# Kernel tuning notes

Measured on AMD Instinct MI355X. Metric: run time of the kernel, lower is better.

The kernel has to match this reference:

```python
import jax, jax.numpy as jnp
import numpy as np


def setup_inputs() -> dict:
    key = jax.random.key(0)
    ks = jax.random.split(key, 7)
    OUT, IN, K = 4096, 4096, 2048
    U_STORED, VT_STORED = 512, 1024  # int(0.5*(K//2+1)), int(0.5*(IN//2+1))
    return {
        "x": jax.random.normal(ks[0], (1024, IN), dtype=jnp.float32),
        "U_real": jax.random.normal(ks[1], (OUT, U_STORED), dtype=jnp.float32) * 0.01,
        "U_imag": jax.random.normal(ks[2], (OUT, U_STORED), dtype=jnp.float32) * 0.01,
        "S": jax.random.normal(ks[3], (K,), dtype=jnp.float32) * 0.02,
        "Vt_real": jax.random.normal(ks[4], (K, VT_STORED), dtype=jnp.float32) * 0.01,
        "Vt_imag": jax.random.normal(ks[5], (K, VT_STORED), dtype=jnp.float32) * 0.01,
        "bias": jnp.zeros((OUT,), dtype=jnp.float32),
    }


def _decompress(coeffs_real, coeffs_imag, n):
    # Zero-pad truncated rfft coefficients back to n//2+1, then inverse rfft.
    c = jax.lax.complex(coeffs_real, coeffs_imag)
    num_unique = n // 2 + 1
    pad = num_unique - c.shape[-1]
    if pad > 0:
        c = jnp.pad(c, ((0, 0), (0, pad)))
    elif pad < 0:
        c = c[..., :num_unique]
    return jnp.fft.irfft(c, n=n, axis=-1)


def reference(x, U_real, U_imag, S, Vt_real, Vt_imag, bias):
    k_rank = S.shape[0]
    in_features = x.shape[-1]
    U = _decompress(U_real, U_imag, k_rank)            # (out, k)
    Vh = _decompress(Vt_real, Vt_imag, in_features)    # (k, in)
    W = (U * S[None, :]) @ Vh                          # (out, in) reconstructed weight
    return x @ W.T + bias                              # F.linear(x, W, bias)
```

## Files before the change

### kernel.cpp

```cpp
#include <hip/hip_runtime.h>
#include <math.h>
#include <stdint.h>

#define PI2 6.28318530717958647692f

typedef __bf16 bf16x8 __attribute__((ext_vector_type(8)));
typedef float f32x4 __attribute__((ext_vector_type(4)));

typedef __attribute__((address_space(1))) const void gvoid_t;
typedef __attribute__((address_space(3))) void lvoid_t;

__device__ __forceinline__ void g2l16(const void* g, void* l) {
    __builtin_amdgcn_global_load_lds(
        reinterpret_cast<gvoid_t*>(reinterpret_cast<uintptr_t>(g)),
        reinterpret_cast<lvoid_t*>(reinterpret_cast<uintptr_t>(l)),
        16, 0, 0);
}

__device__ __forceinline__ short f2bf(float f) {
    unsigned u = __float_as_uint(f);
    u += 0x7FFFu + ((u >> 16) & 1u);
    return (short)(u >> 16);
}

__device__ __forceinline__ unsigned pack2bf(float a, float b) {
    return (unsigned)(unsigned short)f2bf(a) |
           ((unsigned)(unsigned short)f2bf(b) << 16);
}

__device__ __forceinline__ float bflo(unsigned v) { return __uint_as_float(v << 16); }
__device__ __forceinline__ float bfhi(unsigned v) { return __uint_as_float(v & 0xFFFF0000u); }

__device__ __forceinline__ int xcd_swizzle(int blk, int G) {
    return (blk & 7) * (G >> 3) + (blk >> 3);
}

__global__ __launch_bounds__(256) void aux_all8(
    const float* __restrict__ x,
    const float* __restrict__ Ur, const float* __restrict__ Ui,
    const float* __restrict__ S,
    const float* __restrict__ Vr, const float* __restrict__ Vi,
    short* __restrict__ xe, short* __restrict__ xo,
    short* __restrict__ B1f, short* __restrict__ Vcat,
    short* __restrict__ B2, short* __restrict__ Ucat)
{
    unsigned i8 = (blockIdx.x * 256u + threadIdx.x) * 8u;
    if (i8 < 2097152u) {
        unsigned i = i8;
        int r = i >> 11, j0 = i & 2047;
        const float* xr = x + (size_t)r * 4096 + j0;
        float4 a0 = ((const float4*)xr)[0], a1 = ((const float4*)xr)[1];
        float4 b0 = ((const float4*)(xr + 2048))[0],
               b1 = ((const float4*)(xr + 2048))[1];
        uint4 oe = {pack2bf(a0.x + b0.x, a0.y + b0.y),
                    pack2bf(a0.z + b0.z, a0.w + b0.w),
                    pack2bf(a1.x + b1.x, a1.y + b1.y),
                    pack2bf(a1.z + b1.z, a1.w + b1.w)};
        *(uint4*)(xe + i) = oe;
        uint4 oo = {pack2bf(a0.x - b0.x, a0.y - b0.y),
                    pack2bf(a0.z - b0.z, a0.w - b0.w),
                    pack2bf(a1.x - b1.x, a1.y - b1.y),
                    pack2bf(a1.z - b1.z, a1.w - b1.w)};
        *(uint4*)(xo + i) = oo;
    } else if (i8 < 6291456u) {
        unsigned i = i8 - 2097152u;
        int r = i >> 11, j0 = i & 2047;
        const float inv_n = 1.0f / 4096.0f;
        float v[8];
        if (r < 512) {
            if (r == 0) {
                #pragma unroll
                for (int u = 0; u < 8; ++u) v[u] = inv_n;
            } else {
                #pragma unroll
                for (int u = 0; u < 8; ++u) {
                    int t = (r * (j0 + u)) & 2047;
                    v[u] = 2.0f * inv_n * cosf((float)t * (PI2 / 2048.0f));
                }
            }
        } else if (r < 1024) {
            int m = r - 512;
            #pragma unroll
            for (int u = 0; u < 8; ++u) {
                int t = (m * (j0 + u)) & 2047;
                v[u] = -2.0f * inv_n * sinf((float)t * (PI2 / 2048.0f));
            }
        } else if (r < 1536) {
            int c = 2 * (r - 1024) + 1;
            #pragma unroll
            for (int u = 0; u < 8; ++u) {
                int t = (c * (j0 + u)) & 4095;
                v[u] = 2.0f * inv_n * cosf((float)t * (PI2 / 4096.0f));
            }
        } else {
            int m = 2 * (r - 1536) + 1;
            #pragma unroll
            for (int u = 0; u < 8; ++u) {
                int t = (m * (j0 + u)) & 4095;
                v[u] = -2.0f * inv_n * sinf((float)t * (PI2 / 4096.0f));
            }
        }
        uint4 o = {pack2bf(v[0], v[1]), pack2bf(v[2], v[3]),
                   pack2bf(v[4], v[5]), pack2bf(v[6], v[7])};
        *(uint4*)(B1f + i) = o;
    } else if (i8 < 10485760u) {
        unsigned i = i8 - 6291456u;
        int k = i >> 11, c0 = i & 2047;
        int cls = c0 >> 9, cc0 = c0 & 511;
        const float* src = ((cls & 1) ? Vi : Vr) + (size_t)k * 1024 + 2 * cc0;
        float4 q0 = ((const float4*)src)[0];
        float4 q1 = ((const float4*)src)[1];
        float4 q2 = ((const float4*)src)[2];
        float4 q3 = ((const float4*)src)[3];
        float v[8];
        if ((cls >> 1) == 0) {
            v[0] = q0.x; v[1] = q0.z; v[2] = q1.x; v[3] = q1.z;
            v[4] = q2.x; v[5] = q2.z; v[6] = q3.x; v[7] = q3.z;
        } else {
            v[0] = q0.y; v[1] = q0.w; v[2] = q1.y; v[3] = q1.w;
            v[4] = q2.y; v[5] = q2.w; v[6] = q3.y; v[7] = q3.w;
        }
        uint4 o = {pack2bf(v[0], v[1]), pack2bf(v[2], v[3]),
                   pack2bf(v[4], v[5]), pack2bf(v[6], v[7])};
        *(uint4*)(Vcat + i) = o;
    } else if (i8 < 12582912u) {
        unsigned i = i8 - 10485760u;
        int p = i >> 11, k0 = i & 2047;
        float4 s0 = *(const float4*)(S + k0);
        float4 s1 = *(const float4*)(S + k0 + 4);
        float sv[8] = {s0.x, s0.y, s0.z, s0.w, s1.x, s1.y, s1.z, s1.w};
        const float inv_n = 1.0f / 2048.0f;
        float v[8];
        if (p == 0) {
            #pragma unroll
            for (int u = 0; u < 8; ++u) v[u] = inv_n * sv[u];
        } else if (p < 512) {
            #pragma unroll
            for (int u = 0; u < 8; ++u) {
                int t = (p * (k0 + u)) & 2047;
                v[u] = 2.0f * inv_n * cosf((float)t * (PI2 / 2048.0f)) * sv[u];
            }
        } else {
            int q = p - 512;
            #pragma unroll
            for (int u = 0; u < 8; ++u) {
                int t = (q * (k0 + u)) & 2047;
                v[u] = -2.0f * inv_n * sinf((float)t * (PI2 / 2048.0f)) * sv[u];
            }
        }
        uint4 o = {pack2bf(v[0], v[1]), pack2bf(v[2], v[3]),
                   pack2bf(v[4], v[5]), pack2bf(v[6], v[7])};
        *(uint4*)(B2 + i) = o;
    } else {
        unsigned i = i8 - 12582912u;
        int o_ = i >> 10, c = i & 1023;
        const float* src = (c < 512) ? (Ur + (size_t)o_ * 512 + c)
                                     : (Ui + (size_t)o_ * 512 + (c - 512));
        float4 a = ((const float4*)src)[0], b = ((const float4*)src)[1];
        uint4 o = {pack2bf(a.x, a.y), pack2bf(a.z, a.w),
                   pack2bf(b.x, b.y), pack2bf(b.z, b.w)};
        *(uint4*)(Ucat + i) = o;
    }
}

__device__ __forceinline__ void tile_core(
    const short* __restrict__ A, int lda,
    const short* __restrict__ B, int ldb, int K,
    short* As, short* Bs, int bm, int bn, f32x4 (&acc)[4][4])
{
    const int tid  = threadIdx.x;
    const int wave = tid >> 6;
    const int lane = tid & 63;
    const int wm   = (wave >> 1) << 6;
    const int wn   = (wave & 1) << 6;
    const int l16  = lane & 15;
    const int quad = lane >> 4;
    const int rk   = l16 & 7;

    int aoff[4], boff[4], loff[4];
    #pragma unroll
    for (int p = 0; p < 4; ++p) {
        int L   = p * 256 + wave * 64 + lane;
        int row = L >> 3;
        int swz = (L & 7) ^ (row & 7);
        aoff[p] = (bm + row) * lda + swz * 8;
        boff[p] = (bn + row) * ldb + swz * 8;
        loff[p] = L * 8;
    }

    for (int k0 = 0; k0 < K; k0 += 64) {
        __syncthreads();
        #pragma unroll
        for (int p = 0; p < 4; ++p) g2l16(A + aoff[p] + k0, As + loff[p]);
        #pragma unroll
        for (int p = 0; p < 4; ++p) g2l16(B + boff[p] + k0, Bs + loff[p]);
        __syncthreads();

        #pragma unroll
        for (int h = 0; h < 2; ++h) {
            const int cs8 = ((((h << 2) | quad) ^ rk) << 3);
            bf16x8 b[4];
            #pragma unroll
            for (int nt = 0; nt < 4; ++nt)
                b[nt] = *(const bf16x8*)(Bs + (wn + nt * 16 + l16) * 64 + cs8);
            #pragma unroll
            for (int mt = 0; mt < 4; ++mt) {
                bf16x8 a = *(const bf16x8*)(As + (wm + mt * 16 + l16) * 64 + cs8);
                #pragma unroll
                for (int nt = 0; nt < 4; ++nt)
                    acc[mt][nt] = __builtin_amdgcn_mfma_f32_16x16x32_bf16(
                        a, b[nt], acc[mt][nt], 0, 0, 0);
            }
        }
    }
}

__device__ __forceinline__ void store_tile_bf16(
    f32x4 (&acc)[4][4], short* __restrict__ C, int ldc, int bm, int bn)
{
    const int tid  = threadIdx.x;
    const int wave = tid >> 6;
    const int lane = tid & 63;
    const int wm   = (wave >> 1) << 6;
    const int wn   = (wave & 1) << 6;
    const int l16  = lane & 15;
    const int quad = lane >> 4;
    #pragma unroll
    for (int nt = 0; nt < 4; ++nt) {
        int col = bn + wn + nt * 16 + l16;
        #pragma unroll
        for (int mt = 0; mt < 4; ++mt) {
            int rowb = bm + wm + mt * 16 + quad * 4;
            #pragma unroll
            for (int r = 0; r < 4; ++r)
                C[(size_t)(rowb + r) * ldc + col] = f2bf(acc[mt][nt][r]);
        }
    }
}

__device__ __forceinline__ void store_frag(
    f32x4 (&acc)[4][4], short* __restrict__ planeTile)
{
    uint4* p = (uint4*)planeTile;
    const int tid = threadIdx.x;
    #pragma unroll
    for (int c = 0; c < 8; ++c) {
        int nt = c >> 1, mt0 = (c & 1) * 2;
        uint4 o = {pack2bf(acc[mt0][nt][0],     acc[mt0][nt][1]),
                   pack2bf(acc[mt0][nt][2],     acc[mt0][nt][3]),
                   pack2bf(acc[mt0 + 1][nt][0], acc[mt0 + 1][nt][1]),
                   pack2bf(acc[mt0 + 1][nt][2], acc[mt0 + 1][nt][3])};
        p[c * 256 + tid] = o;
    }
}

template <bool OUT_F32>
__device__ __forceinline__ void reduce_unit(
    const short* __restrict__ P, size_t planeU4, int SK,
    int tile, int c, int tilesX, void* __restrict__ Out, int ldc,
    const float* __restrict__ bias)
{
    const int bm = (tile / tilesX) << 7;
    const int bn = (tile % tilesX) << 7;
    const int tid  = threadIdx.x;
    const int wave = tid >> 6;
    const int lane = tid & 63;
    const int wm   = (wave >> 1) << 6;
    const int wn   = (wave & 1) << 6;
    const int l16  = lane & 15;
    const int quad = lane >> 4;
    const int nt   = c >> 1, mt0 = (c & 1) * 2;

    const uint4* P4 = (const uint4*)P;
    const size_t base = (size_t)tile * 2048 + (size_t)c * 256 + tid;
    float f[8] = {0, 0, 0, 0, 0, 0, 0, 0};
    for (int z = 0; z < SK; ++z) {
        uint4 v = P4[(size_t)z * planeU4 + base];
        f[0] += bflo(v.x); f[1] += bfhi(v.x);
        f[2] += bflo(v.y); f[3] += bfhi(v.y);
        f[4] += bflo(v.z); f[5] += bfhi(v.z);
        f[6] += bflo(v.w); f[7] += bfhi(v.w);
    }
    const int col = bn + wn + nt * 16 + l16;
    float bv = 0.f;
    if (OUT_F32) bv = bias[col];
    #pragma unroll
    for (int j = 0; j < 8; ++j) {
        int mt  = mt0 + (j >> 2);
        int row = bm + wm + mt * 16 + quad * 4 + (j & 3);
        if (OUT_F32)
            ((float*)Out)[(size_t)row * ldc + col] = f[j] + bv;
        else
            ((short*)Out)[(size_t)row * ldc + col] = f2bf(f[j]);
    }
}

__global__ __launch_bounds__(256, 4) void gemm_s1f(
    const short* __restrict__ xe, const short* __restrict__ xo,
    const short* __restrict__ B1f, short* __restrict__ P)
{
    __shared__ __align__(16) short As[128 * 64];
    __shared__ __align__(16) short Bs[128 * 64];

    f32x4 acc[4][4];
    #pragma unroll
    for (int i = 0; i < 4; ++i)
        #pragma unroll
        for (int j = 0; j < 4; ++j)
            acc[i][j] = (f32x4){0.f, 0.f, 0.f, 0.f};

    const int u    = xcd_swizzle((int)blockIdx.x, (int)gridDim.x);
    const int z    = u >> 7;
    const int tile = u & 127;
    const int tx   = tile & 15, ty = tile >> 4;
    const bool odd = (tx & 8) != 0;
    const short* A = (odd ? xo : xe) + (size_t)z * 512;
    const short* B = B1f + (odd ? (size_t)1024 * 2048 : 0) + (size_t)z * 512;
    const int bm   = ty << 7;
    const int bn   = (tx & 7) << 7;

    tile_core(A, 2048, B, 2048, 512, As, Bs, bm, bn, acc);
    store_frag(acc, P + (size_t)z * 2097152 + (size_t)tile * 16384);
}

__global__ __launch_bounds__(256, 4) void gemm_sk_frag(
    const short* __restrict__ A, int lda,
    const short* __restrict__ B, int ldb,
    short* __restrict__ P, size_t planeShorts, int Kpart,
    int tileShift, int tilesXShift)
{
    __shared__ __align__(16) short As[128 * 64];
    __shared__ __align__(16) short Bs[128 * 64];

    f32x4 acc[4][4];
    #pragma unroll
    for (int i = 0; i < 4; ++i)
        #pragma unroll
        for (int j = 0; j < 4; ++j)
            acc[i][j] = (f32x4){0.f, 0.f, 0.f, 0.f};

    const int u    = xcd_swizzle((int)blockIdx.x, (int)gridDim.x);
    const int z    = u >> tileShift;
    const int tile = u & ((1 << tileShift) - 1);
    const int bm   = (tile >> tilesXShift) << 7;
    const int bn   = (tile & ((1 << tilesXShift) - 1)) << 7;

    tile_core(A + (size_t)z * Kpart, lda, B + (size_t)z * Kpart, ldb, Kpart,
              As, Bs, bm, bn, acc);
    store_frag(acc, P + (size_t)z * planeShorts + (size_t)tile * 16384);
}

template <bool OUT_F32>
__global__ __launch_bounds__(256) void reduce_frag(
    const short* __restrict__ P, size_t planeShorts, int SK,
    int tilesX, void* __restrict__ Out, int ldc,
    const float* __restrict__ bias)
{
    reduce_unit<OUT_F32>(P, planeShorts >> 3, SK,
                         (int)(blockIdx.x >> 3), (int)(blockIdx.x & 7),
                         tilesX, Out, ldc, bias);
}

template <bool OUT_F32>
__global__ __launch_bounds__(256, 4) void gemm_direct(
    const short* __restrict__ A, int lda,
    const short* __restrict__ B, int ldb,
    void* __restrict__ Cv, int ldc,
    const float* __restrict__ bias, int K)
{
    __shared__ __align__(16) short As[128 * 64];
    __shared__ __align__(16) short Bs[128 * 64];

    f32x4 acc[4][4];
    #pragma unroll
    for (int i = 0; i < 4; ++i)
        #pragma unroll
        for (int j = 0; j < 4; ++j)
            acc[i][j] = (f32x4){0.f, 0.f, 0.f, 0.f};

    const int bm = blockIdx.y << 7;
    const int bn = blockIdx.x << 7;
    tile_core(A, lda, B, ldb, K, As, Bs, bm, bn, acc);

    const int tid  = threadIdx.x;
    const int wave = tid >> 6;
    const int lane = tid & 63;
    const int wm   = (wave >> 1) << 6;
    const int wn   = (wave & 1) << 6;
    const int l16  = lane & 15;
    const int quad = lane >> 4;

    if (OUT_F32) {
        float* C = (float*)Cv;
        #pragma unroll
        for (int nt = 0; nt < 4; ++nt) {
            int col = bn + wn + nt * 16 + l16;
            float bv = bias ? bias[col] : 0.f;
            #pragma unroll
            for (int mt = 0; mt < 4; ++mt) {
                int rowb = bm + wm + mt * 16 + quad * 4;
                #pragma unroll
                for (int r = 0; r < 4; ++r)
                    C[(size_t)(rowb + r) * ldc + col] = acc[mt][nt][r] + bv;
            }
        }
    } else {
        store_tile_bf16(acc, (short*)Cv, ldc, bm, bn);
    }
}

extern "C" void kernel_launch(void* const* d_in, const int* in_sizes, int n_in,
                              void* d_out, int out_size, void* d_ws, size_t ws_size,
                              hipStream_t stream) {
    const float* x    = (const float*)d_in[0];
    const float* Ur   = (const float*)d_in[1];
    const float* Ui   = (const float*)d_in[2];
    const float* S    = (const float*)d_in[3];
    const float* Vr   = (const float*)d_in[4];
    const float* Vi   = (const float*)d_in[5];
    const float* bias = (const float*)d_in[6];
    float* out = (float*)d_out;

    short* ws   = (short*)d_ws;
    short* xe   = ws;
    short* xo   = xe   + (size_t)1024 * 2048;
    short* B1f  = xo   + (size_t)1024 * 2048;
    short* Vcat = B1f  + (size_t)2048 * 2048;
    short* B2   = Vcat + (size_t)2048 * 2048;
    short* Ucat = B2   + (size_t)1024 * 2048;
    short* Xp   = Ucat + (size_t)4096 * 1024;
    short* T1   = Xp   + (size_t)1024 * 2048;
    short* Gm   = T1   + (size_t)1024 * 2048;
    short* Pp   = Gm   + (size_t)1024 * 1024;

    const size_t need = (size_t)((char*)(Pp + (size_t)8388608) - (char*)d_ws);

    aux_all8<<<dim3(8192), 256, 0, stream>>>(
        x, Ur, Ui, S, Vr, Vi, xe, xo, B1f, Vcat, B2, Ucat);

    if (ws_size >= need) {
        gemm_s1f<<<dim3(512), 256, 0, stream>>>(xe, xo, B1f, Pp);
        reduce_frag<false><<<dim3(1024), 256, 0, stream>>>(
            Pp, (size_t)2097152, 4, 16, Xp, 2048, nullptr);

        gemm_sk_frag<<<dim3(512), 256, 0, stream>>>(
            Xp, 2048, Vcat, 2048, Pp, (size_t)2097152, 512, 7, 4);
        reduce_frag<false><<<dim3(1024), 256, 0, stream>>>(
            Pp, (size_t)2097152, 4, 16, T1, 2048, nullptr);

        gemm_sk_frag<<<dim3(512), 256, 0, stream>>>(
            T1, 2048, B2, 2048, Pp, (size_t)1048576, 256, 6, 3);
        reduce_frag<false><<<dim3(512), 256, 0, stream>>>(
            Pp, (size_t)1048576, 8, 8, Gm, 1024, nullptr);

        gemm_sk_frag<<<dim3(512), 256, 0, stream>>>(
            Gm, 1024, Ucat, 1024, Pp, (size_t)4194304, 512, 8, 5);
        reduce_frag<true><<<dim3(2048), 256, 0, stream>>>(
            Pp, (size_t)4194304, 2, 32, out, 4096, bias);
    } else {
        gemm_direct<false><<<dim3(8, 8), 256, 0, stream>>>(
            xe, 2048, B1f, 2048, Xp, 2048, nullptr, 2048);
        gemm_direct<false><<<dim3(8, 8), 256, 0, stream>>>(
            xo, 2048, B1f + (size_t)1024 * 2048, 2048, Xp + 1024, 2048,
            nullptr, 2048);
        gemm_direct<false><<<dim3(16, 8), 256, 0, stream>>>(
            Xp, 2048, Vcat, 2048, T1, 2048, nullptr, 2048);
        gemm_direct<false><<<dim3(8, 8), 256, 0, stream>>>(
            T1, 2048, B2, 2048, Gm, 1024, nullptr, 2048);
        gemm_direct<true><<<dim3(32, 8), 256, 0, stream>>>(
            Gm, 1024, Ucat, 1024, out, 4096, bias, 1024);
    }
}
```

Before: 190.5 us.

## Split aux prep, overlap weight prep with first GEMM, atomic split-K final GEMM

```diff
diff --git a/kernel.cpp b/kernel.cpp
--- a/kernel.cpp
+++ b/kernel.cpp
@@ -35,18 +35,14 @@
     return (blk & 7) * (G >> 3) + (blk >> 3);
 }
 
-__global__ __launch_bounds__(256) void aux_all8(
+__global__ __launch_bounds__(256) void aux1(
     const float* __restrict__ x,
-    const float* __restrict__ Ur, const float* __restrict__ Ui,
-    const float* __restrict__ S,
-    const float* __restrict__ Vr, const float* __restrict__ Vi,
     short* __restrict__ xe, short* __restrict__ xo,
-    short* __restrict__ B1f, short* __restrict__ Vcat,
-    short* __restrict__ B2, short* __restrict__ Ucat)
-{
-    unsigned i8 = (blockIdx.x * 256u + threadIdx.x) * 8u;
-    if (i8 < 2097152u) {
-        unsigned i = i8;
+    short* __restrict__ B1f, float* __restrict__ outz)
+{
+    int b = blockIdx.x;
+    if (b < 1024) {
+        unsigned i = (b * 256u + threadIdx.x) * 8u;
         int r = i >> 11, j0 = i & 2047;
         const float* xr = x + (size_t)r * 4096 + j0;
         float4 a0 = ((const float4*)xr)[0], a1 = ((const float4*)xr)[1];
@@ -62,8 +58,8 @@
                     pack2bf(a1.x - b1.x, a1.y - b1.y),
                     pack2bf(a1.z - b1.z, a1.w - b1.w)};
         *(uint4*)(xo + i) = oo;
-    } else if (i8 < 6291456u) {
-        unsigned i = i8 - 2097152u;
+    } else if (b < 3072) {
+        unsigned i = ((b - 1024) * 256u + threadIdx.x) * 8u;
         int r = i >> 11, j0 = i & 2047;
         const float inv_n = 1.0f / 4096.0f;
         float v[8];
@@ -103,8 +99,24 @@
         uint4 o = {pack2bf(v[0], v[1]), pack2bf(v[2], v[3]),
                    pack2bf(v[4], v[5]), pack2bf(v[6], v[7])};
         *(uint4*)(B1f + i) = o;
-    } else if (i8 < 10485760u) {
-        unsigned i = i8 - 6291456u;
+    } else {
+        size_t idx = ((size_t)(b - 3072) * 256 + threadIdx.x) * 16;
+        uint4 zz = {0, 0, 0, 0};
+        *(uint4*)(outz + idx)     = zz;
+        *(uint4*)(outz + idx + 8) = zz;
+    }
+}
+
+__device__ __forceinline__ void aux2_body(
+    int b2,
+    const float* __restrict__ Ur, const float* __restrict__ Ui,
+    const float* __restrict__ S,
+    const float* __restrict__ Vr, const float* __restrict__ Vi,
+    short* __restrict__ Vcat, short* __restrict__ B2,
+    short* __restrict__ Ucat)
+{
+    if (b2 < 2048) {
+        unsigned i = (b2 * 256u + threadIdx.x) * 8u;
         int k = i >> 11, c0 = i & 2047;
         int cls = c0 >> 9, cc0 = c0 & 511;
         const float* src = ((cls & 1) ? Vi : Vr) + (size_t)k * 1024 + 2 * cc0;
@@ -123,8 +135,8 @@
         uint4 o = {pack2bf(v[0], v[1]), pack2bf(v[2], v[3]),
                    pack2bf(v[4], v[5]), pack2bf(v[6], v[7])};
         *(uint4*)(Vcat + i) = o;
-    } else if (i8 < 12582912u) {
-        unsigned i = i8 - 10485760u;
+    } else if (b2 < 3072) {
+        unsigned i = ((b2 - 2048) * 256u + threadIdx.x) * 8u;
         int p = i >> 11, k0 = i & 2047;
         float4 s0 = *(const float4*)(S + k0);
         float4 s1 = *(const float4*)(S + k0 + 4);
@@ -152,7 +164,7 @@
                    pack2bf(v[4], v[5]), pack2bf(v[6], v[7])};
         *(uint4*)(B2 + i) = o;
     } else {
-        unsigned i = i8 - 12582912u;
+        unsigned i = ((b2 - 3072) * 256u + threadIdx.x) * 8u;
         int o_ = i >> 10, c = i & 1023;
         const float* src = (c < 512) ? (Ur + (size_t)o_ * 512 + c)
                                      : (Ui + (size_t)o_ * 512 + (c - 512));
@@ -161,6 +173,16 @@
                    pack2bf(b.x, b.y), pack2bf(b.z, b.w)};
         *(uint4*)(Ucat + i) = o;
     }
+}
+
+__global__ __launch_bounds__(256) void aux2_only(
+    const float* __restrict__ Ur, const float* __restrict__ Ui,
+    const float* __restrict__ S,
+    const float* __restrict__ Vr, const float* __restrict__ Vi,
+    short* __restrict__ Vcat, short* __restrict__ B2,
+    short* __restrict__ Ucat)
+{
+    aux2_body((int)blockIdx.x, Ur, Ui, S, Vr, Vi, Vcat, B2, Ucat);
 }
 
 __device__ __forceinline__ void tile_core(
@@ -295,10 +317,20 @@
     }
 }
 
-__global__ __launch_bounds__(256, 4) void gemm_s1f(
+__global__ __launch_bounds__(256, 4) void gemm_s1f_aux(
     const short* __restrict__ xe, const short* __restrict__ xo,
-    const short* __restrict__ B1f, short* __restrict__ P)
-{
+    const short* __restrict__ B1f, short* __restrict__ P,
+    const float* __restrict__ Ur, const float* __restrict__ Ui,
+    const float* __restrict__ S,
+    const float* __restrict__ Vr, const float* __restrict__ Vi,
+    short* __restrict__ Vcat, short* __restrict__ B2,
+    short* __restrict__ Ucat)
+{
+    if (blockIdx.x >= 512) {
+        aux2_body((int)blockIdx.x - 512, Ur, Ui, S, Vr, Vi, Vcat, B2, Ucat);
+        return;
+    }
+
     __shared__ __align__(16) short As[128 * 64];
     __shared__ __align__(16) short Bs[128 * 64];
 
@@ -309,7 +341,7 @@
         for (int j = 0; j < 4; ++j)
             acc[i][j] = (f32x4){0.f, 0.f, 0.f, 0.f};
 
-    const int u    = xcd_swizzle((int)blockIdx.x, (int)gridDim.x);
+    const int u    = xcd_swizzle((int)blockIdx.x, 512);
     const int z    = u >> 7;
     const int tile = u & 127;
     const int tx   = tile & 15, ty = tile >> 4;
@@ -359,6 +391,54 @@
     reduce_unit<OUT_F32>(P, planeShorts >> 3, SK,
                          (int)(blockIdx.x >> 3), (int)(blockIdx.x & 7),
                          tilesX, Out, ldc, bias);
+}
+
+__global__ __launch_bounds__(256, 4) void gemm_sk_atomic(
+    const short* __restrict__ A, int lda,
+    const short* __restrict__ B, int ldb, int Kpart,
+    int tileShift, int tilesXShift,
+    float* __restrict__ Out, int ldc, const float* __restrict__ bias)
+{
+    __shared__ __align__(16) short As[128 * 64];
+    __shared__ __align__(16) short Bs[128 * 64];
+
+    f32x4 acc[4][4];
+    #pragma unroll
+    for (int i = 0; i < 4; ++i)
+        #pragma unroll
+        for (int j = 0; j < 4; ++j)
+            acc[i][j] = (f32x4){0.f, 0.f, 0.f, 0.f};
+
+    const int u    = xcd_swizzle((int)blockIdx.x, (int)gridDim.x);
+    const int z    = u >> tileShift;
+    const int tile = u & ((1 << tileShift) - 1);
+    const int bm   = (tile >> tilesXShift) << 7;
+    const int bn   = (tile & ((1 << tilesXShift) - 1)) << 7;
+
+    tile_core(A + (size_t)z * Kpart, lda, B + (size_t)z * Kpart, ldb, Kpart,
+              As, Bs, bm, bn, acc);
+
+    const int tid  = threadIdx.x;
+    const int wave = tid >> 6;
+    const int lane = tid & 63;
+    const int wm   = (wave >> 1) << 6;
+    const int wn   = (wave & 1) << 6;
+    const int l16  = lane & 15;
+    const int quad = lane >> 4;
+
+    #pragma unroll
+    for (int nt = 0; nt < 4; ++nt) {
+        int col = bn + wn + nt * 16 + l16;
+        float bv = (z == 0) ? bias[col] : 0.f;
+        #pragma unroll
+        for (int mt = 0; mt < 4; ++mt) {
+            int rowb = bm + wm + mt * 16 + quad * 4;
+            #pragma unroll
+            for (int r = 0; r < 4; ++r)
+                atomicAdd(&Out[(size_t)(rowb + r) * ldc + col],
+                          acc[mt][nt][r] + bv);
+        }
+    }
 }
 
 template <bool OUT_F32>
@@ -435,11 +515,11 @@
 
     const size_t need = (size_t)((char*)(Pp + (size_t)8388608) - (char*)d_ws);
 
-    aux_all8<<<dim3(8192), 256, 0, stream>>>(
-        x, Ur, Ui, S, Vr, Vi, xe, xo, B1f, Vcat, B2, Ucat);
+    aux1<<<dim3(4096), 256, 0, stream>>>(x, xe, xo, B1f, out);
 
     if (ws_size >= need) {
-        gemm_s1f<<<dim3(512), 256, 0, stream>>>(xe, xo, B1f, Pp);
+        gemm_s1f_aux<<<dim3(5632), 256, 0, stream>>>(
+            xe, xo, B1f, Pp, Ur, Ui, S, Vr, Vi, Vcat, B2, Ucat);
         reduce_frag<false><<<dim3(1024), 256, 0, stream>>>(
             Pp, (size_t)2097152, 4, 16, Xp, 2048, nullptr);
 
@@ -453,11 +533,11 @@
         reduce_frag<false><<<dim3(512), 256, 0, stream>>>(
             Pp, (size_t)1048576, 8, 8, Gm, 1024, nullptr);
 
-        gemm_sk_frag<<<dim3(512), 256, 0, stream>>>(
-            Gm, 1024, Ucat, 1024, Pp, (size_t)4194304, 512, 8, 5);
-        reduce_frag<true><<<dim3(2048), 256, 0, stream>>>(
-            Pp, (size_t)4194304, 2, 32, out, 4096, bias);
+        gemm_sk_atomic<<<dim3(512), 256, 0, stream>>>(
+            Gm, 1024, Ucat, 1024, 512, 8, 5, out, 4096, bias);
     } else {
+        aux2_only<<<dim3(5120), 256, 0, stream>>>(
+            Ur, Ui, S, Vr, Vi, Vcat, B2, Ucat);
         gemm_direct<false><<<dim3(8, 8), 256, 0, stream>>>(
             xe, 2048, B1f, 2048, Xp, 2048, nullptr, 2048);
         gemm_direct<false><<<dim3(8, 8), 256, 0, stream>>>(
```

Result: slower. 203.6 us (+6.9%).

## Double-buffer LDS tiles to overlap global loads with MFMA compute

Applied to the files above, without the earlier changes.

```diff
diff --git a/kernel.cpp b/kernel.cpp
--- a/kernel.cpp
+++ b/kernel.cpp
@@ -188,30 +188,44 @@
         loff[p] = L * 8;
     }
 
+    #pragma unroll
+    for (int p = 0; p < 4; ++p) g2l16(A + aoff[p], As + loff[p]);
+    #pragma unroll
+    for (int p = 0; p < 4; ++p) g2l16(B + boff[p], Bs + loff[p]);
+    __syncthreads();
+
+    int cur = 0;
     for (int k0 = 0; k0 < K; k0 += 64) {
-        __syncthreads();
-        #pragma unroll
-        for (int p = 0; p < 4; ++p) g2l16(A + aoff[p] + k0, As + loff[p]);
-        #pragma unroll
-        for (int p = 0; p < 4; ++p) g2l16(B + boff[p] + k0, Bs + loff[p]);
-        __syncthreads();
-
+        const int nxt = cur ^ 1;
+        if (k0 + 64 < K) {
+            #pragma unroll
+            for (int p = 0; p < 4; ++p)
+                g2l16(A + aoff[p] + k0 + 64, As + nxt * 8192 + loff[p]);
+            #pragma unroll
+            for (int p = 0; p < 4; ++p)
+                g2l16(B + boff[p] + k0 + 64, Bs + nxt * 8192 + loff[p]);
+        }
+
+        const short* Asc = As + cur * 8192;
+        const short* Bsc = Bs + cur * 8192;
         #pragma unroll
         for (int h = 0; h < 2; ++h) {
             const int cs8 = ((((h << 2) | quad) ^ rk) << 3);
             bf16x8 b[4];
             #pragma unroll
             for (int nt = 0; nt < 4; ++nt)
-                b[nt] = *(const bf16x8*)(Bs + (wn + nt * 16 + l16) * 64 + cs8);
+                b[nt] = *(const bf16x8*)(Bsc + (wn + nt * 16 + l16) * 64 + cs8);
             #pragma unroll
             for (int mt = 0; mt < 4; ++mt) {
-                bf16x8 a = *(const bf16x8*)(As + (wm + mt * 16 + l16) * 64 + cs8);
+                bf16x8 a = *(const bf16x8*)(Asc + (wm + mt * 16 + l16) * 64 + cs8);
                 #pragma unroll
                 for (int nt = 0; nt < 4; ++nt)
                     acc[mt][nt] = __builtin_amdgcn_mfma_f32_16x16x32_bf16(
                         a, b[nt], acc[mt][nt], 0, 0, 0);
             }
         }
+        __syncthreads();
+        cur = nxt;
     }
 }
 
@@ -295,12 +309,12 @@
     }
 }
 
-__global__ __launch_bounds__(256, 4) void gemm_s1f(
+__global__ __launch_bounds__(256, 2) void gemm_s1f(
     const short* __restrict__ xe, const short* __restrict__ xo,
     const short* __restrict__ B1f, short* __restrict__ P)
 {
-    __shared__ __align__(16) short As[128 * 64];
-    __shared__ __align__(16) short Bs[128 * 64];
+    __shared__ __align__(16) short As[2 * 128 * 64];
+    __shared__ __align__(16) short Bs[2 * 128 * 64];
 
     f32x4 acc[4][4];
     #pragma unroll
@@ -323,14 +337,14 @@
     store_frag(acc, P + (size_t)z * 2097152 + (size_t)tile * 16384);
 }
 
-__global__ __launch_bounds__(256, 4) void gemm_sk_frag(
+__global__ __launch_bounds__(256, 2) void gemm_sk_frag(
     const short* __restrict__ A, int lda,
     const short* __restrict__ B, int ldb,
     short* __restrict__ P, size_t planeShorts, int Kpart,
     int tileShift, int tilesXShift)
 {
-    __shared__ __align__(16) short As[128 * 64];
-    __shared__ __align__(16) short Bs[128 * 64];
+    __shared__ __align__(16) short As[2 * 128 * 64];
+    __shared__ __align__(16) short Bs[2 * 128 * 64];
 
     f32x4 acc[4][4];
     #pragma unroll
@@ -362,14 +376,14 @@
 }
 
 template <bool OUT_F32>
-__global__ __launch_bounds__(256, 4) void gemm_direct(
+__global__ __launch_bounds__(256, 2) void gemm_direct(
     const short* __restrict__ A, int lda,
     const short* __restrict__ B, int ldb,
     void* __restrict__ Cv, int ldc,
     const float* __restrict__ bias, int K)
 {
-    __shared__ __align__(16) short As[128 * 64];
-    __shared__ __align__(16) short Bs[128 * 64];
+    __shared__ __align__(16) short As[2 * 128 * 64];
+    __shared__ __align__(16) short Bs[2 * 128 * 64];
 
     f32x4 acc[4][4];
     #pragma unroll
```

Result: faster. 185.2 us (-2.8%).
